# Optimization experiments

Measured on AMD Instinct MI355X. Metric: run time of the kernel, lower is better.

## Reference

```python
import jax, jax.numpy as jnp
import numpy as np

D_MODEL = 1024
N_HEADS = 16
HEAD_SIZE = D_MODEL // N_HEADS
D_FF = 4096
EPS = 1e-6


def _layernorm(x, g, b):
    # Faithful to source: (x + mean) / (std + eps), unbiased std (torch default)
    mean = jnp.mean(x, axis=-1, keepdims=True)
    std = jnp.std(x, axis=-1, keepdims=True, ddof=1)
    return g * ((x + mean) / (std + EPS)) + b


def setup_inputs() -> dict:
    key = jax.random.key(0)
    ks = jax.random.split(key, 12)
    s = lambda fan_in: 1.0 / np.sqrt(fan_in)
    x = jax.random.normal(ks[0], (4, 2048, D_MODEL), dtype=jnp.float32)
    Wq = jax.random.uniform(ks[1], (N_HEADS, D_MODEL, HEAD_SIZE), jnp.float32, -s(D_MODEL), s(D_MODEL))
    Wk = jax.random.uniform(ks[2], (N_HEADS, D_MODEL, HEAD_SIZE), jnp.float32, -s(D_MODEL), s(D_MODEL))
    Wv = jax.random.uniform(ks[3], (N_HEADS, D_MODEL, HEAD_SIZE), jnp.float32, -s(D_MODEL), s(D_MODEL))
    Wo = jax.random.uniform(ks[4], (D_MODEL, D_MODEL), jnp.float32, -s(D_MODEL), s(D_MODEL))
    bo = jax.random.uniform(ks[5], (D_MODEL,), jnp.float32, -s(D_MODEL), s(D_MODEL))
    W1 = jax.random.uniform(ks[6], (D_MODEL, D_FF), jnp.float32, -s(D_MODEL), s(D_MODEL))
    b1 = jax.random.uniform(ks[7], (D_FF,), jnp.float32, -s(D_MODEL), s(D_MODEL))
    W2 = jax.random.uniform(ks[8], (D_FF, D_MODEL), jnp.float32, -s(D_FF), s(D_FF))
    b2 = jax.random.uniform(ks[9], (D_MODEL,), jnp.float32, -s(D_FF), s(D_FF))
    g1 = jnp.ones((D_MODEL,), jnp.float32)
    be1 = jnp.zeros((D_MODEL,), jnp.float32)
    g2 = jnp.ones((D_MODEL,), jnp.float32)
    be2 = jnp.zeros((D_MODEL,), jnp.float32)
    return {"x": x, "Wq": Wq, "Wk": Wk, "Wv": Wv, "Wo": Wo, "bo": bo,
            "W1": W1, "b1": b1, "W2": W2, "b2": b2,
            "g1": g1, "be1": be1, "g2": g2, "be2": be2}


def reference(x, Wq, Wk, Wv, Wo, bo, W1, b1, W2, b2, g1, be1, g2, be2):
    # Multi-head attention; note: source scales by sqrt(d_model), not sqrt(head_size)
    scale = 1.0 / np.sqrt(D_MODEL)
    q = jnp.einsum('bsd,hde->bhse', x, Wq)
    k = jnp.einsum('bsd,hde->bhse', x, Wk)
    v = jnp.einsum('bsd,hde->bhse', x, Wv)
    scores = jnp.einsum('bhse,bhte->bhst', q, k) * scale
    attn = jax.nn.softmax(scores, axis=-1)
    o = jnp.einsum('bhst,bhte->bhse', attn, v)
    B, H, S, E = o.shape
    o = o.transpose(0, 2, 1, 3).reshape(B, S, H * E)  # concat heads
    mha_out = o @ Wo + bo

    h1 = _layernorm(x + mha_out, g1, be1)

    ff = jax.nn.relu(h1 @ W1 + b1) @ W2 + b2
    out = _layernorm(h1 + ff, g2, be2)
    return out
```

## Files before the change

### kernel.cpp

```cpp
#include <hip/hip_runtime.h>

typedef short short8 __attribute__((ext_vector_type(8)));
typedef short short4v __attribute__((ext_vector_type(4)));
typedef float floatx4 __attribute__((ext_vector_type(4)));

#define D_MODEL 1024
#define N_HEADS 16
#define HEAD    64
#define D_FF    4096
#define SEQ     2048
#define BATCH   4
#define TOKENS  (BATCH*SEQ)

__device__ __forceinline__ float b2f(unsigned short u) {
  return __uint_as_float(((unsigned)u) << 16);
}
__device__ __forceinline__ unsigned short f2b(float f) {
  unsigned u = __float_as_uint(f);
  unsigned r = 0x7fffu + ((u >> 16) & 1u);
  return (unsigned short)((u + r) >> 16);
}
__device__ __forceinline__ floatx4 mfma16(short8 a, short8 b, floatx4 c) {
  return __builtin_amdgcn_mfma_f32_16x16x32_bf16(a, b, c, 0, 0, 0);
}
__device__ __forceinline__ void load16_lds(const unsigned short* g, unsigned short* l) {
  __builtin_amdgcn_global_load_lds((const __attribute__((address_space(1))) void*)g,
                                   (__attribute__((address_space(3))) void*)l, 16, 0, 0);
}

__device__ __forceinline__ void transp_body(
    const float* __restrict__ src, unsigned short* __restrict__ dst,
    int R, int C, int bx, int by, float (*t)[65])
{
  int cb = bx * 64, rb = by * 64;
#pragma unroll
  for (int i = 0; i < 16; i++) {
    int idx = i * 256 + threadIdx.x;
    int lr = idx >> 6, lc = idx & 63;
    t[lr][lc] = src[(size_t)(rb + lr) * C + cb + lc];
  }
  __syncthreads();
#pragma unroll
  for (int i = 0; i < 16; i++) {
    int idx = i * 256 + threadIdx.x;
    int lc = idx >> 6, lr = idx & 63;
    dst[(size_t)(cb + lc) * R + rb + lr] = f2b(t[lr][lc]);
  }
}

__global__ __launch_bounds__(256) void prep_kernel(
    const float* __restrict__ x, unsigned short* __restrict__ x_bf,
    const float* __restrict__ Wq, const float* __restrict__ Wk,
    const float* __restrict__ Wv, unsigned short* __restrict__ qkv_bt,
    const float* __restrict__ Wo, unsigned short* __restrict__ wo_bt,
    const float* __restrict__ W1, unsigned short* __restrict__ w1_bt,
    const float* __restrict__ W2, unsigned short* __restrict__ w2_bt)
{
  __shared__ float t[64][65];
  int bid = blockIdx.x;
  if (bid < 8192) {
    int idx = bid * 1024 + threadIdx.x * 4;
    float4 v = *(const float4*)(x + idx);
    short4v o;
    o[0] = (short)f2b(v.x); o[1] = (short)f2b(v.y);
    o[2] = (short)f2b(v.z); o[3] = (short)f2b(v.w);
    *(short4v*)(x_bf + idx) = o;
  } else if (bid < 8960) {
    int by = bid - 8192;
    int xt = by & 15, z = by >> 4;
    int sel = z >> 4, h = z & 15;
    const float* W = (sel == 0) ? Wq : ((sel == 1) ? Wk : Wv);
    const float* src = W + (size_t)h * D_MODEL * HEAD;
    int rb = xt * 64;
#pragma unroll
    for (int i = 0; i < 16; i++) {
      int idx = i * 256 + threadIdx.x;
      int lr = idx >> 6, lc = idx & 63;
      t[lr][lc] = src[(size_t)(rb + lr) * HEAD + lc];
    }
    __syncthreads();
    unsigned short* d0 = qkv_bt + (size_t)(sel * 1024 + h * 64) * D_MODEL;
#pragma unroll
    for (int i = 0; i < 16; i++) {
      int idx = i * 256 + threadIdx.x;
      int lc = idx >> 6, lr = idx & 63;
      d0[(size_t)lc * D_MODEL + rb + lr] = f2b(t[lr][lc]);
    }
  } else if (bid < 9216) {
    int i = bid - 8960;
    transp_body(Wo, wo_bt, 1024, 1024, i & 15, i >> 4, t);
  } else if (bid < 10240) {
    int i = bid - 9216;
    transp_body(W1, w1_bt, 1024, 4096, i & 63, i >> 6, t);
  } else {
    int i = bid - 10240;
    transp_body(W2, w2_bt, 4096, 1024, i & 15, i >> 4, t);
  }
}

__global__ __launch_bounds__(256, 2) void gemm128(
    const unsigned short* __restrict__ A, const unsigned short* __restrict__ BT,
    const float* __restrict__ biasf, const float* __restrict__ residf,
    const unsigned short* __restrict__ residb, void* __restrict__ outp,
    int M, int N, int K, int epi)
{
  __shared__ unsigned short a_sh[2 * 128 * 32];
  __shared__ unsigned short b_sh[2 * 128 * 32];

  const int tid  = threadIdx.x;
  const int lane = tid & 63;
  const int wave = tid >> 6;
  const int quad = lane >> 4;
  const int l15  = lane & 15;
  const int wm   = wave & 1;
  const int wn   = wave >> 1;

  const int lin = blockIdx.y * gridDim.x + blockIdx.x;
  const int xcd = lin & 7, j = lin >> 3;
  const int m0 = (xcd * 8 + (j & 7)) * 128;
  const int n0 = (j >> 3) * 128;

  const int rA = tid >> 2;
  const int kc = (tid & 3) * 8;
  const unsigned short* ag0 = A  + (size_t)(m0 + rA) * K + kc;
  const unsigned short* ag1 = A  + (size_t)(m0 + rA + 64) * K + kc;
  const unsigned short* bg0 = BT + (size_t)(n0 + rA) * K + kc;
  const unsigned short* bg1 = BT + (size_t)(n0 + rA + 64) * K + kc;
  unsigned short* la0 = a_sh + wave * 512;
  unsigned short* la1 = a_sh + 2048 + wave * 512;
  unsigned short* lb0 = b_sh + wave * 512;
  unsigned short* lb1 = b_sh + 2048 + wave * 512;

  floatx4 acc[4][4] = {};

  for (int k0 = 0; k0 < K; k0 += 64) {
    __syncthreads();
    load16_lds(ag0 + k0, la0);
    load16_lds(ag1 + k0, la1);
    load16_lds(bg0 + k0, lb0);
    load16_lds(bg1 + k0, lb1);
    load16_lds(ag0 + k0 + 32, la0 + 4096);
    load16_lds(ag1 + k0 + 32, la1 + 4096);
    load16_lds(bg0 + k0 + 32, lb0 + 4096);
    load16_lds(bg1 + k0 + 32, lb1 + 4096);
    __syncthreads();
#pragma unroll
    for (int h = 0; h < 2; h++) {
      short8 aF[4], bF[4];
#pragma unroll
      for (int i = 0; i < 4; i++)
        aF[i] = *(const short8*)(a_sh + h * 4096 + (wm * 64 + i * 16 + l15) * 32 + quad * 8);
#pragma unroll
      for (int i = 0; i < 4; i++)
        bF[i] = *(const short8*)(b_sh + h * 4096 + (wn * 64 + i * 16 + l15) * 32 + quad * 8);
#pragma unroll
      for (int mi = 0; mi < 4; mi++)
#pragma unroll
        for (int ni = 0; ni < 4; ni++)
          acc[mi][ni] = mfma16(aF[mi], bF[ni], acc[mi][ni]);
    }
  }

#pragma unroll
  for (int mi = 0; mi < 4; mi++) {
#pragma unroll
    for (int ni = 0; ni < 4; ni++) {
      const int col = n0 + wn * 64 + ni * 16 + l15;
      const int row0 = m0 + wm * 64 + mi * 16 + quad * 4;
      if (epi == 0) {
        int sel = col >> 10;
        int cc = col & 1023;
        int h = cc >> 6, e = cc & 63;
        int b = row0 >> 11, s0 = row0 & 2047;
        if (sel < 2) {
          unsigned short* base = (unsigned short*)outp + (size_t)sel * 8388608;
#pragma unroll
          for (int r = 0; r < 4; r++) {
            float v2 = (sel == 0) ? acc[mi][ni][r] * 0.03125f : acc[mi][ni][r];
            base[((size_t)((b * N_HEADS + h) * SEQ + (s0 + r))) * HEAD + e] = f2b(v2);
          }
        } else {
          unsigned short* base = (unsigned short*)outp + (size_t)2 * 8388608;
          short4v pk;
#pragma unroll
          for (int r = 0; r < 4; r++) pk[r] = (short)f2b(acc[mi][ni][r]);
          *(short4v*)(base + ((size_t)((b * N_HEADS + h) * HEAD + e)) * SEQ + s0) = pk;
        }
      } else if (epi == 1) {
#pragma unroll
        for (int r = 0; r < 4; r++)
          ((float*)outp)[(size_t)(row0 + r) * N + col] =
              acc[mi][ni][r] + biasf[col] + residf[(size_t)(row0 + r) * N + col];
      } else if (epi == 2) {
#pragma unroll
        for (int r = 0; r < 4; r++)
          ((unsigned short*)outp)[(size_t)(row0 + r) * N + col] =
              f2b(fmaxf(acc[mi][ni][r] + biasf[col], 0.0f));
      } else {
#pragma unroll
        for (int r = 0; r < 4; r++)
          ((float*)outp)[(size_t)(row0 + r) * N + col] =
              acc[mi][ni][r] + biasf[col] + b2f(residb[(size_t)(row0 + r) * N + col]);
      }
    }
  }
}

__global__ __launch_bounds__(256) void attn_kernel(
    const unsigned short* __restrict__ q, const unsigned short* __restrict__ k,
    const unsigned short* __restrict__ vt, unsigned short* __restrict__ o)
{
  const int bh = blockIdx.y;
  const int qt = blockIdx.x;
  const int tid = threadIdx.x, lane = tid & 63, wave = tid >> 6;
  const int quad = lane >> 4, l15 = lane & 15;
  const size_t base = (size_t)bh * SEQ * HEAD;

  __shared__ unsigned short k_sh[64 * 64];
  __shared__ unsigned short vT_sh[64 * 64];
  __shared__ unsigned short p_sh[4 * 32 * 72];
  unsigned short* pw = p_sh + wave * 32 * 72;

  short8 qf[2][2];
#pragma unroll
  for (int mj = 0; mj < 2; mj++) {
    const unsigned short* qp =
        q + base + (size_t)(qt * 128 + wave * 32 + mj * 16 + l15) * HEAD;
    qf[mj][0] = *(const short8*)(qp + quad * 8);
    qf[mj][1] = *(const short8*)(qp + 32 + quad * 8);
  }

  floatx4 oacc[2][4] = {};
  float rs[2] = {0.0f, 0.0f};

  const int r8 = lane >> 3, slot = lane & 7;

  for (int kt = 0; kt < SEQ / 64; kt++) {
    __syncthreads();
#pragma unroll
    for (int i = 0; i < 2; i++) {
      int t = wave * 16 + i * 8 + r8;
      int cg = slot ^ (t & 7);
      load16_lds(k + base + (size_t)(kt * 64 + t) * HEAD + cg * 8,
                 k_sh + (wave * 16 + i * 8) * 64);
      load16_lds(vt + base + (size_t)t * SEQ + kt * 64 + cg * 8,
                 vT_sh + (wave * 16 + i * 8) * 64);
    }
    __syncthreads();

#pragma unroll
    for (int ti = 0; ti < 4; ti++) {
      int t = ti * 16 + l15;
      short8 kf0 = *(const short8*)(k_sh + t * 64 + ((quad ^ (t & 7)) * 8));
      short8 kf1 = *(const short8*)(k_sh + t * 64 + (((4 + quad) ^ (t & 7)) * 8));
      floatx4 s0 = {0.f, 0.f, 0.f, 0.f}, s1 = {0.f, 0.f, 0.f, 0.f};
      s0 = mfma16(kf0, qf[0][0], s0);
      s0 = mfma16(kf1, qf[0][1], s0);
      s1 = mfma16(kf0, qf[1][0], s1);
      s1 = mfma16(kf1, qf[1][1], s1);
#pragma unroll
      for (int mj = 0; mj < 2; mj++) {
        floatx4 s = mj ? s1 : s0;
        float p0 = __expf(s[0]), p1 = __expf(s[1]);
        float p2 = __expf(s[2]), p3 = __expf(s[3]);
        rs[mj] += (p0 + p1) + (p2 + p3);
        uint2 u;
        u.x = __builtin_amdgcn_perm(__float_as_uint(p1), __float_as_uint(p0), 0x07060302u);
        u.y = __builtin_amdgcn_perm(__float_as_uint(p3), __float_as_uint(p2), 0x07060302u);
        *(uint2*)(pw + (mj * 16 + l15) * 72 + ti * 16 + quad * 4) = u;
      }
    }

#pragma unroll
    for (int mj = 0; mj < 2; mj++) {
      short8 pf0 = *(const short8*)(pw + (mj * 16 + l15) * 72 + quad * 8);
      short8 pf1 = *(const short8*)(pw + (mj * 16 + l15) * 72 + 32 + quad * 8);
#pragma unroll
      for (int ni = 0; ni < 4; ni++) {
        int e = ni * 16 + l15;
        short8 bv0 = *(const short8*)(vT_sh + e * 64 + ((quad ^ (e & 7)) * 8));
        short8 bv1 = *(const short8*)(vT_sh + e * 64 + (((4 + quad) ^ (e & 7)) * 8));
        oacc[mj][ni] = mfma16(pf0, bv0, oacc[mj][ni]);
        oacc[mj][ni] = mfma16(pf1, bv1, oacc[mj][ni]);
      }
    }
  }

#pragma unroll
  for (int mj = 0; mj < 2; mj++) {
    rs[mj] += __shfl_xor(rs[mj], 16, 64);
    rs[mj] += __shfl_xor(rs[mj], 32, 64);
  }

  const int b = bh >> 4, h = bh & 15;
#pragma unroll
  for (int mj = 0; mj < 2; mj++)
#pragma unroll
    for (int r = 0; r < 4; r++) {
      int s = qt * 128 + wave * 32 + mj * 16 + quad * 4 + r;
      float inv = 1.0f / __shfl(rs[mj], quad * 4 + r, 64);
#pragma unroll
      for (int ni = 0; ni < 4; ni++)
        o[((size_t)(b * SEQ + s)) * D_MODEL + h * HEAD + ni * 16 + l15] =
            f2b(oacc[mj][ni][r] * inv);
    }
}

__global__ __launch_bounds__(256) void ln_kernel(
    const float* __restrict__ in, const float* __restrict__ g,
    const float* __restrict__ be, void* __restrict__ outp, int write_bf16)
{
  const int row = blockIdx.x * 4 + (threadIdx.x >> 6);
  const int lane = threadIdx.x & 63;
  const float* xp = in + (size_t)row * D_MODEL;
  float4 xv[4];
  float s = 0.0f, ss = 0.0f;
#pragma unroll
  for (int j = 0; j < 4; j++) {
    xv[j] = *(const float4*)(xp + j * 256 + lane * 4);
    s += (xv[j].x + xv[j].y) + (xv[j].z + xv[j].w);
    ss += (xv[j].x * xv[j].x + xv[j].y * xv[j].y) +
          (xv[j].z * xv[j].z + xv[j].w * xv[j].w);
  }
#pragma unroll
  for (int m = 1; m < 64; m <<= 1) {
    s += __shfl_xor(s, m, 64);
    ss += __shfl_xor(ss, m, 64);
  }
  float mean = s * (1.0f / 1024.0f);
  float var = fmaxf((ss - 1024.0f * mean * mean) * (1.0f / 1023.0f), 0.0f);
  float inv = 1.0f / (sqrtf(var) + 1e-6f);
#pragma unroll
  for (int j = 0; j < 4; j++) {
    int c = j * 256 + lane * 4;
    float4 g4 = *(const float4*)(g + c);
    float4 b4 = *(const float4*)(be + c);
    float y0 = g4.x * ((xv[j].x + mean) * inv) + b4.x;
    float y1 = g4.y * ((xv[j].y + mean) * inv) + b4.y;
    float y2 = g4.z * ((xv[j].z + mean) * inv) + b4.z;
    float y3 = g4.w * ((xv[j].w + mean) * inv) + b4.w;
    if (write_bf16) {
      short4v o4;
      o4[0] = (short)f2b(y0); o4[1] = (short)f2b(y1);
      o4[2] = (short)f2b(y2); o4[3] = (short)f2b(y3);
      *(short4v*)((unsigned short*)outp + (size_t)row * D_MODEL + c) = o4;
    } else {
      float4 o4 = {y0, y1, y2, y3};
      *(float4*)((float*)outp + (size_t)row * D_MODEL + c) = o4;
    }
  }
}

extern "C" void kernel_launch(void* const* d_in, const int* in_sizes, int n_in,
                              void* d_out, int out_size, void* d_ws, size_t ws_size,
                              hipStream_t stream)
{
  const float* x   = (const float*)d_in[0];
  const float* Wq  = (const float*)d_in[1];
  const float* Wk  = (const float*)d_in[2];
  const float* Wv  = (const float*)d_in[3];
  const float* Wo  = (const float*)d_in[4];
  const float* bo  = (const float*)d_in[5];
  const float* W1  = (const float*)d_in[6];
  const float* b1  = (const float*)d_in[7];
  const float* W2  = (const float*)d_in[8];
  const float* b2  = (const float*)d_in[9];
  const float* g1  = (const float*)d_in[10];
  const float* be1 = (const float*)d_in[11];
  const float* g2  = (const float*)d_in[12];
  const float* be2 = (const float*)d_in[13];
  float* out = (float*)d_out;

  unsigned short* ws     = (unsigned short*)d_ws;
  unsigned short* w1_bt  = ws;
  unsigned short* w2_bt  = ws + 4194304;
  unsigned short* qkv_bt = ws + 8388608;
  unsigned short* wo_bt  = ws + 11534336;
  unsigned short* x_bf   = ws + 12582912;
  unsigned short* qws    = ws + 20971520;
  unsigned short* kws    = ws + 29360128;
  unsigned short* vws    = ws + 37748736;
  unsigned short* ows    = x_bf;
  float*          r1     = (float*)(ws + 20971520);
  unsigned short* h1_bf  = x_bf;
  unsigned short* ff1    = ws + 20971520;

  dim3 blk(256);

  prep_kernel<<<11264, blk, 0, stream>>>(x, x_bf, Wq, Wk, Wv, qkv_bt,
                                         Wo, wo_bt, W1, w1_bt, W2, w2_bt);

  gemm128<<<dim3(3072 / 128, TOKENS / 128), blk, 0, stream>>>(
      x_bf, qkv_bt, nullptr, nullptr, nullptr, qws, TOKENS, 3072, 1024, 0);
  attn_kernel<<<dim3(SEQ / 128, BATCH * N_HEADS), blk, 0, stream>>>(qws, kws, vws, ows);
  gemm128<<<dim3(1024 / 128, TOKENS / 128), blk, 0, stream>>>(
      ows, wo_bt, bo, x, nullptr, r1, TOKENS, 1024, 1024, 1);
  ln_kernel<<<TOKENS / 4, blk, 0, stream>>>(r1, g1, be1, h1_bf, 1);
  gemm128<<<dim3(4096 / 128, TOKENS / 128), blk, 0, stream>>>(
      h1_bf, w1_bt, b1, nullptr, nullptr, ff1, TOKENS, 4096, 1024, 2);
  gemm128<<<dim3(1024 / 128, TOKENS / 128), blk, 0, stream>>>(
      ff1, w2_bt, b2, nullptr, h1_bf, out, TOKENS, 1024, 4096, 3);
  ln_kernel<<<TOKENS / 4, blk, 0, stream>>>(out, g2, be2, out, 0);
}
```

Measured before the change: 501.9 us.

## Add 256x256-tile 8-wave pipelined GEMM for QKV and FFN1 projections

Adds a new gemm256 kernel that uses 512 threads and 256x256 output tiles. It double-buffers direct-to-LDS loads with XOR-swizzled layouts and splits each K step into four phases, interleaving MFMA work with the next tile's loads under barriers and s_setprio. It also remaps blocks across XCDs so neighbouring M tiles share each die's L2. This kernel replaces gemm128 for the QKV projection and the first FFN GEMM, aiming for more data reuse per tile and better latency hiding. The costs are much higher register and LDS use, fewer blocks per grid, and a hand-tuned wait-count schedule that must match the exact number of outstanding loads.

```diff
diff --git a/kernel.cpp b/kernel.cpp
--- a/kernel.cpp
+++ b/kernel.cpp
@@ -206,6 +206,185 @@
   }
 }
 
+__global__ __launch_bounds__(512, 2) void gemm256(
+    const unsigned short* __restrict__ A, const unsigned short* __restrict__ BT,
+    const float* __restrict__ biasf, void* __restrict__ outp,
+    int M, int N, int K, int epi)
+{
+  __shared__ unsigned short a_sh[2 * 256 * 64];
+  __shared__ unsigned short b_sh[2 * 256 * 64];
+
+  const int tid  = threadIdx.x;
+  const int lane = tid & 63;
+  const int wave = tid >> 6;
+  const int quad = lane >> 4;
+  const int l15  = lane & 15;
+  const int wm   = wave >> 2;
+  const int wn   = wave & 3;
+
+  const int lin = blockIdx.y * gridDim.x + blockIdx.x;
+  const int xcd = lin & 7, j = lin >> 3;
+  const int m0 = (xcd * 4 + (j & 3)) * 256;
+  const int n0 = (j >> 2) * 256;
+
+  const int u  = tid >> 3;
+  const int sc = (tid & 7) ^ (u & 7);
+  const unsigned short* a_src = A  + (size_t)(m0 + u) * K + sc * 8;
+  const int borig = ((u >> 5) * 64) + (u & 31);
+  const unsigned short* b_src = BT + (size_t)(n0 + borig) * K + sc * 8;
+  unsigned short* a_dst = a_sh + wave * 512;
+  unsigned short* b_dst = b_sh + wave * 512;
+
+#define SA(T, Rc)  load16_lds(a_src + (size_t)(Rc) * K + (T) * 64, \
+                              a_dst + ((T) & 1) * 16384 + (Rc) * 64)
+#define SB(T, Rb, Radd) load16_lds(b_src + (size_t)(Radd) * K + (T) * 64, \
+                              b_dst + ((T) & 1) * 16384 + (Rb) * 64)
+#define STG_A0(T) do { SA(T, 0);   SA(T, 128); } while (0)
+#define STG_A1(T) do { SA(T, 64);  SA(T, 192); } while (0)
+#define STG_B0(T) do { SB(T, 0, 0);    SB(T, 64, 128); } while (0)
+#define STG_B1(T) do { SB(T, 128, 32); SB(T, 192, 160); } while (0)
+
+  floatx4 acc[8][4] = {};
+  short8 aF[4][2];
+  short8 bF[2][2][2];
+  const unsigned short* ash = a_sh;
+  const unsigned short* bsh = b_sh;
+
+#define LDA(QM) \
+  _Pragma("unroll") for (int mi = 0; mi < 4; mi++) \
+  _Pragma("unroll") for (int kh = 0; kh < 2; kh++) \
+    aF[mi][kh] = *(const short8*)(ash + (wm * 128 + (QM) * 64 + mi * 16 + l15) * 64 \
+                                  + (((kh * 4 + quad) ^ (l15 & 7)) * 8));
+#define LDB(QN) \
+  _Pragma("unroll") for (int ni = 0; ni < 2; ni++) \
+  _Pragma("unroll") for (int kh = 0; kh < 2; kh++) \
+    bF[QN][ni][kh] = *(const short8*)(bsh + ((QN) * 128 + wn * 32 + ni * 16 + l15) * 64 \
+                                      + (((kh * 4 + quad) ^ (l15 & 7)) * 8));
+#define MM(QM, QN) \
+  _Pragma("unroll") for (int mi = 0; mi < 4; mi++) \
+  _Pragma("unroll") for (int ni = 0; ni < 2; ni++) { \
+    acc[(QM) * 4 + mi][(QN) * 2 + ni] = \
+        mfma16(aF[mi][0], bF[QN][ni][0], acc[(QM) * 4 + mi][(QN) * 2 + ni]); \
+    acc[(QM) * 4 + mi][(QN) * 2 + ni] = \
+        mfma16(aF[mi][1], bF[QN][ni][1], acc[(QM) * 4 + mi][(QN) * 2 + ni]); \
+  }
+#define PH_MID(VMW) \
+  asm volatile("s_waitcnt vmcnt(" #VMW ")" ::: "memory"); \
+  __builtin_amdgcn_s_barrier(); \
+  asm volatile("s_waitcnt lgkmcnt(0)" ::: "memory"); \
+  __builtin_amdgcn_sched_barrier(0); \
+  __builtin_amdgcn_s_setprio(1);
+#define PH_END() \
+  __builtin_amdgcn_s_setprio(0); \
+  __builtin_amdgcn_s_barrier();
+
+  const int NT = K >> 6;
+
+  STG_A0(0); STG_B0(0); STG_A1(0); STG_B1(0); STG_A0(1); STG_B0(1);
+  asm volatile("s_waitcnt vmcnt(8)" ::: "memory");
+  __builtin_amdgcn_s_barrier();
+
+  for (int t = 0; t < NT - 2; ++t) {
+    ash = a_sh + (t & 1) * 16384;
+    bsh = b_sh + (t & 1) * 16384;
+
+    LDA(0) LDB(0)
+    STG_A1(t + 1);
+    PH_MID(6) MM(0, 0) PH_END();
+
+    LDB(1)
+    STG_B1(t + 1);
+    PH_MID(6) MM(0, 1) PH_END();
+
+    LDA(1)
+    STG_A0(t + 2);
+    PH_MID(6) MM(1, 0) PH_END();
+
+    STG_B0(t + 2);
+    PH_MID(6) MM(1, 1) PH_END();
+  }
+  {
+    const int t = NT - 2;
+    ash = a_sh + (t & 1) * 16384;
+    bsh = b_sh + (t & 1) * 16384;
+
+    LDA(0) LDB(0)
+    STG_A1(t + 1);
+    PH_MID(6) MM(0, 0) PH_END();
+
+    LDB(1)
+    STG_B1(t + 1);
+    PH_MID(6) MM(0, 1) PH_END();
+
+    LDA(1)
+    PH_MID(6) MM(1, 0) PH_END();
+
+    PH_MID(4) MM(1, 1) PH_END();
+  }
+  {
+    const int t = NT - 1;
+    ash = a_sh + (t & 1) * 16384;
+    bsh = b_sh + (t & 1) * 16384;
+
+    LDA(0) LDB(0)
+    PH_MID(0) MM(0, 0) PH_END();
+
+    LDB(1)
+    PH_MID(0) MM(0, 1) PH_END();
+
+    LDA(1)
+    PH_MID(0) MM(1, 0) PH_END();
+
+    PH_MID(0) MM(1, 1) PH_END();
+  }
+
+#undef SA
+#undef SB
+#undef STG_A0
+#undef STG_A1
+#undef STG_B0
+#undef STG_B1
+#undef LDA
+#undef LDB
+#undef MM
+#undef PH_MID
+#undef PH_END
+
+#pragma unroll
+  for (int mi = 0; mi < 8; mi++) {
+#pragma unroll
+    for (int ni = 0; ni < 4; ni++) {
+      const int col = n0 + wn * 64 + ni * 16 + l15;
+      const int row0 = m0 + wm * 128 + mi * 16 + quad * 4;
+      if (epi == 0) {
+        int sel = col >> 10;
+        int cc = col & 1023;
+        int h = cc >> 6, e = cc & 63;
+        int b = row0 >> 11, s0 = row0 & 2047;
+        if (sel < 2) {
+          unsigned short* base = (unsigned short*)outp + (size_t)sel * 8388608;
+#pragma unroll
+          for (int r = 0; r < 4; r++) {
+            float v2 = (sel == 0) ? acc[mi][ni][r] * 0.03125f : acc[mi][ni][r];
+            base[((size_t)((b * N_HEADS + h) * SEQ + (s0 + r))) * HEAD + e] = f2b(v2);
+          }
+        } else {
+          unsigned short* base = (unsigned short*)outp + (size_t)2 * 8388608;
+          short4v pk;
+#pragma unroll
+          for (int r = 0; r < 4; r++) pk[r] = (short)f2b(acc[mi][ni][r]);
+          *(short4v*)(base + ((size_t)((b * N_HEADS + h) * HEAD + e)) * SEQ + s0) = pk;
+        }
+      } else {
+#pragma unroll
+        for (int r = 0; r < 4; r++)
+          ((unsigned short*)outp)[(size_t)(row0 + r) * N + col] =
+              f2b(fmaxf(acc[mi][ni][r] + biasf[col], 0.0f));
+      }
+    }
+  }
+}
+
 __global__ __launch_bounds__(256) void attn_kernel(
     const unsigned short* __restrict__ q, const unsigned short* __restrict__ k,
     const unsigned short* __restrict__ vt, unsigned short* __restrict__ o)
@@ -390,14 +569,14 @@
   prep_kernel<<<11264, blk, 0, stream>>>(x, x_bf, Wq, Wk, Wv, qkv_bt,
                                          Wo, wo_bt, W1, w1_bt, W2, w2_bt);
 
-  gemm128<<<dim3(3072 / 128, TOKENS / 128), blk, 0, stream>>>(
-      x_bf, qkv_bt, nullptr, nullptr, nullptr, qws, TOKENS, 3072, 1024, 0);
+  gemm256<<<dim3(3072 / 256, TOKENS / 256), dim3(512), 0, stream>>>(
+      x_bf, qkv_bt, nullptr, qws, TOKENS, 3072, 1024, 0);
   attn_kernel<<<dim3(SEQ / 128, BATCH * N_HEADS), blk, 0, stream>>>(qws, kws, vws, ows);
   gemm128<<<dim3(1024 / 128, TOKENS / 128), blk, 0, stream>>>(
       ows, wo_bt, bo, x, nullptr, r1, TOKENS, 1024, 1024, 1);
   ln_kernel<<<TOKENS / 4, blk, 0, stream>>>(r1, g1, be1, h1_bf, 1);
-  gemm128<<<dim3(4096 / 128, TOKENS / 128), blk, 0, stream>>>(
-      h1_bf, w1_bt, b1, nullptr, nullptr, ff1, TOKENS, 4096, 1024, 2);
+  gemm256<<<dim3(4096 / 256, TOKENS / 256), dim3(512), 0, stream>>>(
+      h1_bf, w1_bt, b1, ff1, TOKENS, 4096, 1024, 2);
   gemm128<<<dim3(1024 / 128, TOKENS / 128), blk, 0, stream>>>(
       ff1, w2_bt, b2, nullptr, h1_bf, out, TOKENS, 1024, 4096, 3);
   ln_kernel<<<TOKENS / 4, blk, 0, stream>>>(out, g2, be2, out, 0);
```

Measured after the change: 499.3 us. About the same (-0.5%).
